# Optimization experiments

Measured on AMD Instinct MI355X. Metric: run time of the kernel, lower is better.

Reference implementation:

```python
import jax, jax.numpy as jnp
import numpy as np

EPS = 1e-4  # Coqui LayerNorm (type '1') eps


def _layer_norm_c(x, g, b):
    # x: (B, C, T); normalize over channel dim 1 (Coqui LayerNorm type '1')
    m = jnp.mean(x, axis=1, keepdims=True)
    v = jnp.var(x, axis=1, keepdims=True)
    return (x - m) * jax.lax.rsqrt(v + EPS) * g[None, :, None] + b[None, :, None]


def _s4d(x, log_dt, A_re, A_im, C_re, C_im, D, Wout, bout):
    # S4 (mode='diag' / S4D) layer, transposed=True -> x: (B, H, L)
    L = x.shape[-1]
    dt = jnp.exp(log_dt)[:, None]                       # (H, 1)
    A = A_re + 1j * A_im                                # (H, N2) diagonal SSM
    dtA = A * dt                                        # (H, N2)
    Cd = (C_re + 1j * C_im) * (jnp.exp(dtA) - 1.0) / A  # ZOH-discretized C (B absorbed)
    vand = jnp.exp(dtA[:, :, None] * jnp.arange(L))     # (H, N2, L) Vandermonde
    K = 2.0 * jnp.einsum('hn,hnl->hl', Cd, vand).real   # (H, L) SSM conv kernel
    n = 2 * L                                           # causal conv via FFT
    y = jnp.fft.irfft(jnp.fft.rfft(x, n=n) * jnp.fft.rfft(K, n=n)[None], n=n)[..., :L]
    y = y + D[None, :, None] * x                        # skip connection
    y = jax.nn.gelu(y, approximate=False)               # dropout=0 (eval)
    z = jnp.einsum('oh,bhl->bol', Wout, y) + bout[None, :, None]  # (B, 2H, L)
    a, g = jnp.split(z, 2, axis=1)                      # GLU over channel dim
    return a * jax.nn.sigmoid(g)


def _ffn(x, x_mask, W1, b1, W2, b2):
    # kernel_size=1 feed-forward conv block with masking
    h = jnp.einsum('fh,bhl->bfl', W1, x * x_mask) + b1[None, :, None]
    h = jax.nn.relu(h)
    o = jnp.einsum('of,bfl->bol', W2, h * x_mask) + b2[None, :, None]
    return o * x_mask


def reference(x, x_mask, log_dt, A_re, A_im, C_re, C_im, D, Wout, bout,
              g1, be1, W1, bf1, W2, bf2, g2, be2):
    n_layers = log_dt.shape[0]
    for i in range(n_layers):
        x = x * x_mask
        y = _s4d(x, log_dt[i], A_re[i], A_im[i], C_re[i], C_im[i],
                 D[i], Wout[i], bout[i])
        x = _layer_norm_c(x + y, g1[i], be1[i])
        y = _ffn(x, x_mask, W1[i], bf1[i], W2[i], bf2[i])
        x = _layer_norm_c(x + y, g2[i], be2[i])
    return x * x_mask


def setup_inputs():
    Lyr, B, H, T, N2, HF = 6, 16, 384, 2048, 32, 1536
    key = jax.random.key(0)
    ks = jax.random.split(key, 8)
    x = jax.random.normal(ks[0], (B, H, T), jnp.float32)
    x_mask = jnp.ones((B, 1, T), jnp.float32)
    # stable S4D init: log_dt in [log 1e-3, log 1e-1], A = -1/2 + i*pi*n
    log_dt = (jax.random.uniform(ks[1], (Lyr, H), jnp.float32)
              * (np.log(0.1) - np.log(0.001)) + np.log(0.001))
    A_re = -0.5 * jnp.ones((Lyr, H, N2), jnp.float32)
    A_im = jnp.broadcast_to(np.pi * jnp.arange(N2, dtype=np.float32),
                            (Lyr, H, N2)) * jnp.ones((1,), jnp.float32)
    C_re = jax.random.normal(ks[2], (Lyr, H, N2), jnp.float32) * 0.5 ** 0.5
    C_im = jax.random.normal(ks[3], (Lyr, H, N2), jnp.float32) * 0.5 ** 0.5
    D = jax.random.normal(ks[4], (Lyr, H), jnp.float32)
    Wout = jax.random.normal(ks[5], (Lyr, 2 * H, H), jnp.float32) / np.sqrt(H)
    bout = jnp.zeros((Lyr, 2 * H), jnp.float32)
    g1 = jnp.ones((Lyr, H), jnp.float32)
    be1 = jnp.zeros((Lyr, H), jnp.float32)
    W1 = jax.random.normal(ks[6], (Lyr, HF, H), jnp.float32) / np.sqrt(H)
    bf1 = jnp.zeros((Lyr, HF), jnp.float32)
    W2 = jax.random.normal(ks[7], (Lyr, H, HF), jnp.float32) / np.sqrt(HF)
    bf2 = jnp.zeros((Lyr, H), jnp.float32)
    g2 = jnp.ones((Lyr, H), jnp.float32)
    be2 = jnp.zeros((Lyr, H), jnp.float32)
    return {"x": x, "x_mask": x_mask, "log_dt": log_dt, "A_re": A_re,
            "A_im": A_im, "C_re": C_re, "C_im": C_im, "D": D,
            "Wout": Wout, "bout": bout, "g1": g1, "be1": be1,
            "W1": W1, "bf1": bf1, "W2": W2, "bf2": bf2,
            "g2": g2, "be2": be2}
```

## Files before the change

### kernel.cpp

```cpp
#include <hip/hip_runtime.h>
#include <math.h>

#define Bq 16
#define Hc 384
#define Tt 2048
#define N2 32
#define LYR 6
#define HFq 1536
#define TWOH 768
#define CHUNK 64
#define NCH (Tt/CHUNK)
#define NJ (Bq*NCH)
#define UH (NJ*CHUNK)

typedef __bf16 bf16x8 __attribute__((ext_vector_type(8)));
typedef float floatx4 __attribute__((ext_vector_type(4)));
typedef _Float16 f16_t;
typedef f16_t fp16x8 __attribute__((ext_vector_type(8)));
typedef f16_t fp16x4 __attribute__((ext_vector_type(4)));

__device__ __forceinline__ unsigned short bfbits(float f) {
  union { float f; unsigned u; } x; x.f = f;
  return (unsigned short)((x.u + 0x7FFF + ((x.u >> 16) & 1)) >> 16);
}
__device__ __forceinline__ float bf2f(unsigned short u) {
  union { unsigned u; float f; } x; x.u = ((unsigned)u) << 16; return x.f;
}

__device__ __forceinline__ void gl_lds16(const void* g, void* l) {
  __builtin_amdgcn_global_load_lds(
      (const __attribute__((address_space(1))) void*)g,
      (__attribute__((address_space(3))) void*)l, 16, 0, 0);
}

__global__ void param_kernel(const float* __restrict__ log_dt,
                             const float* __restrict__ A_re, const float* __restrict__ A_im,
                             const float* __restrict__ C_re, const float* __restrict__ C_im,
                             float* __restrict__ wre, float* __restrict__ wim,
                             float* __restrict__ cdre, float* __restrict__ cdim,
                             float* __restrict__ wSre, float* __restrict__ wSim) {
  int idx = blockIdx.x * blockDim.x + threadIdx.x;
  if (idx >= LYR * Hc * N2) return;
  int hn = idx / N2;
  double dt = exp((double)log_dt[hn]);
  double are = (double)A_re[idx], aim = (double)A_im[idx];
  double dre = are * dt, dimv = aim * dt;
  double er = exp(dre);
  double wr = er * cos(dimv), wi_ = er * sin(dimv);
  double den = are * are + aim * aim;
  double nr = wr - 1.0, ni = wi_;
  double qr = (nr * are + ni * aim) / den;
  double qi = (ni * are - nr * aim) / den;
  double cr = (double)C_re[idx], ci = (double)C_im[idx];
  cdre[idx] = (float)(2.0 * (cr * qr - ci * qi));
  cdim[idx] = (float)(2.0 * (cr * qi + ci * qr));
  wre[idx] = (float)wr; wim[idx] = (float)wi_;
  double es = exp(dre * (double)CHUNK);
  wSre[idx] = (float)(es * cos(dimv * (double)CHUNK));
  wSim[idx] = (float)(es * sin(dimv * (double)CHUNK));
}

__global__ void cvt_bf16_kernel(const float* __restrict__ in, unsigned short* __restrict__ out,
                                int n4) {
  int idx = blockIdx.x * 256 + threadIdx.x;
  if (idx >= n4) return;
  float4 v = ((const float4*)in)[idx];
  ushort4 o;
  o.x = bfbits(v.x); o.y = bfbits(v.y); o.z = bfbits(v.z); o.w = bfbits(v.w);
  ((ushort4*)out)[idx] = o;
}

__global__ __launch_bounds__(256) void transpose_fwd(const float* __restrict__ in,
                                                     float* __restrict__ out) {
  __shared__ float tile[32][33];
  int tx = threadIdx.x, ty = threadIdx.y;
  int t0 = blockIdx.x * 32, c0 = blockIdx.y * 32, b = blockIdx.z;
#pragma unroll
  for (int k = 0; k < 4; k++)
    tile[ty + 8 * k][tx] = in[((size_t)(b * Hc + c0 + ty + 8 * k)) * Tt + t0 + tx];
  __syncthreads();
#pragma unroll
  for (int k = 0; k < 4; k++)
    out[((size_t)(b * Tt + t0 + ty + 8 * k)) * Hc + c0 + tx] = tile[tx][ty + 8 * k];
}

__global__ __launch_bounds__(256) void transpose_bwd(const float* __restrict__ in,
                                                     const float* __restrict__ mask,
                                                     float* __restrict__ out) {
  __shared__ float tile[32][33];
  int tx = threadIdx.x, ty = threadIdx.y;
  int t0 = blockIdx.x * 32, c0 = blockIdx.y * 32, b = blockIdx.z;
#pragma unroll
  for (int k = 0; k < 4; k++)
    tile[ty + 8 * k][tx] = in[((size_t)(b * Tt + t0 + ty + 8 * k)) * Hc + c0 + tx];
  __syncthreads();
  float mv = mask[(size_t)b * Tt + t0 + tx];
#pragma unroll
  for (int k = 0; k < 4; k++)
    out[((size_t)(b * Hc + c0 + ty + 8 * k)) * Tt + t0 + tx] = tile[tx][ty + 8 * k] * mv;
}

__global__ __launch_bounds__(256) void pack_u(const float* __restrict__ xT,
                                              const float* __restrict__ mask,
                                              f16_t* __restrict__ U) {
  __shared__ float tile[64][65];
  int tid = threadIdx.x;
  int t0 = blockIdx.x * 64, h0 = blockIdx.y * 64, b = blockIdx.z;
#pragma unroll
  for (int p = 0; p < 4; p++) {
    int idx = p * 256 + tid;
    int row = idx >> 4, c4 = (idx & 15) * 4;
    float4 v = *(const float4*)&xT[((size_t)(b * Tt + t0 + row)) * Hc + h0 + c4];
    float mv = mask[(size_t)b * Tt + t0 + row];
    tile[row][c4] = v.x * mv; tile[row][c4 + 1] = v.y * mv;
    tile[row][c4 + 2] = v.z * mv; tile[row][c4 + 3] = v.w * mv;
  }
  __syncthreads();
#pragma unroll
  for (int p = 0; p < 2; p++) {
    int idx = p * 256 + tid;
    int hr = idx >> 3, g = (idx & 7) * 8;
    fp16x8 o;
#pragma unroll
    for (int i = 0; i < 8; i++) o[i] = (f16_t)tile[g + i][hr];
    *(fp16x8*)&U[(size_t)(h0 + hr) * UH + (size_t)b * Tt + t0 + g] = o;
  }
}

__global__ __launch_bounds__(256) void build_mats(
    const float* __restrict__ wre, const float* __restrict__ wim,
    const float* __restrict__ cdre, const float* __restrict__ cdim,
    f16_t* __restrict__ Ag, f16_t* __restrict__ Wg) {
  __shared__ float pre[65][32], pim[65][32], Kc[64], cdr_s[32], cdi_s[32];
  int h = blockIdx.x, tid = threadIdx.x;
  if (tid < 32) {
    float wr = wre[h * N2 + tid], wi = wim[h * N2 + tid];
    cdr_s[tid] = cdre[h * N2 + tid];
    cdi_s[tid] = cdim[h * N2 + tid];
    float pr = 1.f, pi = 0.f;
    for (int p = 0; p <= 64; p++) {
      pre[p][tid] = pr; pim[p][tid] = pi;
      float nr2 = pr * wr - pi * wi;
      pi = pr * wi + pi * wr;
      pr = nr2;
    }
  }
  __syncthreads();
  if (tid < 64) {
    float s = 0.f;
    for (int n = 0; n < 32; n++)
      s = fmaf(cdr_s[n], pre[tid][n], fmaf(-cdi_s[n], pim[tid][n], s));
    Kc[tid] = s;
  }
  __syncthreads();
  for (int i = tid; i < 64 * 128; i += 256) {
    int m = i >> 7, k = i & 127;
    float v;
    if (k < 64) {
      v = (m >= k) ? Kc[m - k] : 0.f;
    } else {
      int kk = k - 64, n = kk >> 1;
      v = (kk & 1) ? -fmaf(cdr_s[n], pim[m + 1][n], cdi_s[n] * pre[m + 1][n])
                   :  fmaf(cdr_s[n], pre[m + 1][n], -cdi_s[n] * pim[m + 1][n]);
    }
    Ag[(size_t)h * 8192 + i] = (f16_t)v;
  }
  for (int i = tid; i < 64 * 64; i += 256) {
    int m = i >> 6, tau = i & 63, n = m >> 1;
    float v = (m & 1) ? pim[63 - tau][n] : pre[63 - tau][n];
    Wg[(size_t)h * 4096 + i] = (f16_t)v;
  }
}

__global__ __launch_bounds__(256) void gemm_state(const f16_t* __restrict__ U,
                                                  const f16_t* __restrict__ Wg,
                                                  f16_t* __restrict__ St) {
  __shared__ f16_t Aw[64][72];
  __shared__ f16_t Bu[128][72];
  int tid = threadIdx.x;
  int j0 = blockIdx.x * 128, h = blockIdx.y;
#pragma unroll
  for (int p = 0; p < 2; p++) {
    int idx = p * 256 + tid;
    int row = idx >> 3, c8 = (idx & 7) * 8;
    *(fp16x8*)&Aw[row][c8] = *(const fp16x8*)&Wg[(size_t)h * 4096 + row * 64 + c8];
  }
#pragma unroll
  for (int p = 0; p < 4; p++) {
    int idx = p * 256 + tid;
    int row = idx >> 3, c8 = (idx & 7) * 8;
    *(fp16x8*)&Bu[row][c8] =
        *(const fp16x8*)&U[(size_t)h * UH + (size_t)(j0 + row) * CHUNK + c8];
  }
  __syncthreads();
  int wave = tid >> 6, lane = tid & 63, l16 = lane & 15, quad = lane >> 4;
  int m0 = wave * 16;
  floatx4 acc[8];
#pragma unroll
  for (int jt = 0; jt < 8; jt++) acc[jt] = (floatx4){0.f, 0.f, 0.f, 0.f};
#pragma unroll
  for (int kk = 0; kk < 2; kk++) {
    fp16x8 a = *(const fp16x8*)&Aw[m0 + l16][kk * 32 + quad * 8];
#pragma unroll
    for (int jt = 0; jt < 8; jt++) {
      fp16x8 bb = *(const fp16x8*)&Bu[jt * 16 + l16][kk * 32 + quad * 8];
      acc[jt] = __builtin_amdgcn_mfma_f32_16x16x32_f16(a, bb, acc[jt], 0, 0, 0);
    }
  }
#pragma unroll
  for (int jt = 0; jt < 8; jt++) {
    int j = j0 + jt * 16 + l16;
    fp16x4 o;
#pragma unroll
    for (int r = 0; r < 4; r++) o[r] = (f16_t)acc[jt][r];
    *(fp16x4*)&St[(size_t)h * UH + (size_t)j * CHUNK + m0 + quad * 4] = o;
  }
}

__global__ __launch_bounds__(256) void scan_prefix2(
    f16_t* __restrict__ St,
    const float* __restrict__ wSre, const float* __restrict__ wSim) {
  int gid = blockIdx.x * 256 + threadIdx.x;
  if (gid >= Hc * Bq * N2) return;
  int n = gid & 31;
  int b = (gid >> 5) & 15;
  int h = gid >> 9;
  float wr = wSre[h * N2 + n], wi = wSim[h * N2 + n];
  float cr = 0.f, ci = 0.f;
  unsigned* base = (unsigned*)(St + (size_t)h * UH + (size_t)b * Tt + 2 * n);
  for (int c = 0; c < NCH; c++) {
    union { unsigned u; f16_t h2[2]; } in, out;
    in.u = base[c * 32];
    float sre = (float)in.h2[0], sim = (float)in.h2[1];
    out.h2[0] = (f16_t)cr; out.h2[1] = (f16_t)ci;
    base[c * 32] = out.u;
    float c0 = cr;
    cr = fmaf(wr, c0, fmaf(-wi, ci, sre));
    ci = fmaf(wr, ci, fmaf(wi, c0, sim));
  }
}

__global__ __launch_bounds__(256) void gemm_out(
    const f16_t* __restrict__ U, const f16_t* __restrict__ Ag,
    const f16_t* __restrict__ St, const float* __restrict__ Dv,
    unsigned short* __restrict__ Yb) {
  __shared__ f16_t Aa[64][136];
  __shared__ f16_t Bb[128][136];
  int tid = threadIdx.x;
  int j0 = blockIdx.x * 128, h = blockIdx.y;
#pragma unroll
  for (int p = 0; p < 4; p++) {
    int idx = p * 256 + tid;
    int row = idx >> 4, c8 = (idx & 15) * 8;
    *(fp16x8*)&Aa[row][c8] = *(const fp16x8*)&Ag[(size_t)h * 8192 + row * 128 + c8];
  }
#pragma unroll
  for (int p = 0; p < 4; p++) {
    int idx = p * 256 + tid;
    int row = idx >> 3, c8 = (idx & 7) * 8;
    *(fp16x8*)&Bb[row][c8] =
        *(const fp16x8*)&U[(size_t)h * UH + (size_t)(j0 + row) * CHUNK + c8];
    *(fp16x8*)&Bb[row][64 + c8] =
        *(const fp16x8*)&St[(size_t)h * UH + (size_t)(j0 + row) * CHUNK + c8];
  }
  __syncthreads();
  int wave = tid >> 6, lane = tid & 63, l16 = lane & 15, quad = lane >> 4;
  int m0 = wave * 16;
  floatx4 acc[8];
#pragma unroll
  for (int jt = 0; jt < 8; jt++) acc[jt] = (floatx4){0.f, 0.f, 0.f, 0.f};
#pragma unroll
  for (int kk = 0; kk < 4; kk++) {
    fp16x8 a = *(const fp16x8*)&Aa[m0 + l16][kk * 32 + quad * 8];
#pragma unroll
    for (int jt = 0; jt < 8; jt++) {
      fp16x8 bb = *(const fp16x8*)&Bb[jt * 16 + l16][kk * 32 + quad * 8];
      acc[jt] = __builtin_amdgcn_mfma_f32_16x16x32_f16(a, bb, acc[jt], 0, 0, 0);
    }
  }
  float d = Dv[h];
  int tb = m0 + quad * 4;
#pragma unroll
  for (int jt = 0; jt < 8; jt++) {
    int jr = jt * 16 + l16;
    fp16x4 u4 = *(const fp16x4*)&Bb[jr][tb];
    ushort4 o;
#pragma unroll
    for (int r = 0; r < 4; r++) {
      float v = fmaf(d, (float)u4[r], acc[jt][r]);
      v = 0.5f * v * (1.0f + erff(v * 0.70710678118654752f));
      ((unsigned short*)&o)[r] = bfbits(v);
    }
    *(ushort4*)&Yb[(size_t)h * UH + (size_t)(j0 + jr) * CHUNK + tb] = o;
  }
}

__global__ __launch_bounds__(256) void unpack_y(const unsigned short* __restrict__ Yb,
                                                unsigned short* __restrict__ yb) {
  __shared__ unsigned short tile[64][65];
  int tid = threadIdx.x;
  int t0 = blockIdx.x * 64, h0 = blockIdx.y * 64, b = blockIdx.z;
#pragma unroll
  for (int p = 0; p < 2; p++) {
    int idx = p * 256 + tid;
    int hr = idx >> 3, g = (idx & 7) * 8;
    uint4 v = *(const uint4*)&Yb[(size_t)(h0 + hr) * UH + (size_t)b * Tt + t0 + g];
    const unsigned short* s = (const unsigned short*)&v;
#pragma unroll
    for (int i = 0; i < 8; i++) tile[hr][g + i] = s[i];
  }
  __syncthreads();
#pragma unroll
  for (int p = 0; p < 2; p++) {
    int idx = p * 256 + tid;
    int tr = idx >> 3, g = (idx & 7) * 8;
    unsigned short o[8];
#pragma unroll
    for (int i = 0; i < 8; i++) o[i] = tile[g + i][tr];
    *(uint4*)&yb[((size_t)(b * Tt + t0 + tr)) * Hc + h0 + g] = *(uint4*)o;
  }
}

template <int EPI>
__global__ __launch_bounds__(256) void mfma_gemm(
    const __bf16* __restrict__ act, const __bf16* __restrict__ W,
    const float* __restrict__ bias, const float* __restrict__ mask,
    unsigned short* __restrict__ outb, int K, int NOUT) {
  __shared__ __bf16 As[2][128][32];
  __shared__ __bf16 Bs[2][128][32];
  __shared__ __bf16 Bs2[(EPI == 2) ? 2 : 1][(EPI == 2) ? 128 : 1][32];
  int tid = threadIdx.x;
  int b = blockIdx.z;
  int t0 = blockIdx.x * 128, n0 = blockIdx.y * 128;
  int wave = tid >> 6, lane = tid & 63, l16 = lane & 15, quad = lane >> 4;
  int wm = wave >> 1, wn = wave & 1;

  floatx4 acc[4][4];
  floatx4 accg[(EPI == 2) ? 4 : 1][4];
#pragma unroll
  for (int i = 0; i < 4; i++)
#pragma unroll
    for (int j = 0; j < 4; j++) {
      acc[i][j] = (floatx4){0.f, 0.f, 0.f, 0.f};
      if constexpr (EPI == 2) accg[i][j] = (floatx4){0.f, 0.f, 0.f, 0.f};
    }

  int srow = wave * 16 + (lane >> 2);
  int scol = (lane & 3) * 8;
  const __bf16* aSrc = act + ((size_t)(b * Tt + t0 + srow)) * K + scol;
  const __bf16* bSrc = W + (size_t)(n0 + srow) * K + scol;
  const __bf16* gSrc = W + (size_t)(NOUT + n0 + srow) * K + scol;

  auto stage = [&](int buf, int k0) {
#pragma unroll
    for (int r = 0; r < 2; r++) {
      gl_lds16(aSrc + k0 + (size_t)(64 * r) * K, &As[buf][wave * 16 + r * 64][0]);
      gl_lds16(bSrc + k0 + (size_t)(64 * r) * K, &Bs[buf][wave * 16 + r * 64][0]);
      if constexpr (EPI == 2)
        gl_lds16(gSrc + k0 + (size_t)(64 * r) * K, &Bs2[buf][wave * 16 + r * 64][0]);
    }
  };

  stage(0, 0);
  __syncthreads();
  int cur = 0;
  for (int k0 = 0; k0 < K; k0 += 32) {
    if (k0 + 32 < K) stage(cur ^ 1, k0 + 32);
    bf16x8 af[4], bfr[4], gfr[(EPI == 2) ? 4 : 1];
#pragma unroll
    for (int i = 0; i < 4; i++)
      af[i] = *(const bf16x8*)&As[cur][wm * 64 + i * 16 + l16][quad * 8];
#pragma unroll
    for (int j = 0; j < 4; j++) {
      bfr[j] = *(const bf16x8*)&Bs[cur][wn * 64 + j * 16 + l16][quad * 8];
      if constexpr (EPI == 2)
        gfr[j] = *(const bf16x8*)&Bs2[cur][wn * 64 + j * 16 + l16][quad * 8];
    }
#pragma unroll
    for (int i = 0; i < 4; i++)
#pragma unroll
      for (int j = 0; j < 4; j++) {
        acc[i][j] = __builtin_amdgcn_mfma_f32_16x16x32_bf16(af[i], bfr[j], acc[i][j], 0, 0, 0);
        if constexpr (EPI == 2)
          accg[i][j] = __builtin_amdgcn_mfma_f32_16x16x32_bf16(af[i], gfr[j], accg[i][j], 0, 0, 0);
      }
    __syncthreads();
    cur ^= 1;
  }

#pragma unroll
  for (int i = 0; i < 4; i++) {
    int tb = t0 + wm * 64 + i * 16 + quad * 4;
    float mv[4];
    if constexpr (EPI == 1) {
#pragma unroll
      for (int r = 0; r < 4; r++) mv[r] = mask[(size_t)b * Tt + tb + r];
    }
#pragma unroll
    for (int j = 0; j < 4; j++) {
      int n = n0 + wn * 64 + j * 16 + l16;
      float bn = bias[n];
      float bg = (EPI == 2) ? bias[NOUT + n] : 0.f;
#pragma unroll
      for (int r = 0; r < 4; r++) {
        size_t o = ((size_t)(b * Tt + tb + r)) * NOUT + n;
        if constexpr (EPI == 0) {
          outb[o] = bfbits(acc[i][j][r] + bn);
        } else if constexpr (EPI == 1) {
          float v = fmaxf(acc[i][j][r] + bn, 0.f) * mv[r];
          outb[o] = bfbits(v);
        } else {
          float a = acc[i][j][r] + bn;
          float g = accg[i][j][r] + bg;
          outb[o] = bfbits(a / (1.f + expf(-g)));
        }
      }
    }
  }
}

__global__ __launch_bounds__(256) void ln_t(
    const float* __restrict__ in1, const unsigned short* __restrict__ in2b,
    const float* __restrict__ mask, const float* __restrict__ gamma,
    const float* __restrict__ beta, float* __restrict__ out,
    unsigned short* __restrict__ outb, int m1, int m2) {
  int row = blockIdx.x * 4 + (threadIdx.x >> 6);
  int lane = threadIdx.x & 63;
  float mv = mask[row];
  float f1 = m1 ? mv : 1.f;
  float f2 = m2 ? mv : 1.f;
  size_t base = (size_t)row * Hc;
  float v[6], sum = 0.f, sq = 0.f;
#pragma unroll
  for (int j = 0; j < 6; j++) {
    int idx = lane + 64 * j;
    float a = in1[base + idx] * f1 + bf2f(in2b[base + idx]) * f2;
    v[j] = a; sum += a; sq = fmaf(a, a, sq);
  }
#pragma unroll
  for (int off = 32; off >= 1; off >>= 1) {
    sum += __shfl_xor(sum, off, 64);
    sq  += __shfl_xor(sq,  off, 64);
  }
  float m = sum * (1.f / Hc);
  float var = sq * (1.f / Hc) - m * m;
  float rs = rsqrtf(var + 1e-4f);
#pragma unroll
  for (int j = 0; j < 6; j++) {
    int idx = lane + 64 * j;
    float o = (v[j] - m) * rs * gamma[idx] + beta[idx];
    out[base + idx] = o;
    if (outb) outb[base + idx] = bfbits(o * mv);
  }
}

__global__ void diag_kernel(float* out, float v) {
  if (blockIdx.x == 0 && threadIdx.x == 0) out[0] = v;
}

extern "C" void kernel_launch(void* const* d_in, const int* in_sizes, int n_in,
                              void* d_out, int out_size, void* d_ws, size_t ws_size,
                              hipStream_t stream) {
  const float* x_in  = (const float*)d_in[0];
  const float* xmask = (const float*)d_in[1];
  const float* log_dt = (const float*)d_in[2];
  const float* A_re = (const float*)d_in[3];
  const float* A_im = (const float*)d_in[4];
  const float* C_re = (const float*)d_in[5];
  const float* C_im = (const float*)d_in[6];
  const float* Dv   = (const float*)d_in[7];
  const float* Wout = (const float*)d_in[8];
  const float* bout = (const float*)d_in[9];
  const float* g1   = (const float*)d_in[10];
  const float* be1  = (const float*)d_in[11];
  const float* W1   = (const float*)d_in[12];
  const float* bf1  = (const float*)d_in[13];
  const float* W2   = (const float*)d_in[14];
  const float* bf2  = (const float*)d_in[15];
  const float* g2   = (const float*)d_in[16];
  const float* be2  = (const float*)d_in[17];

  const size_t NXf   = (size_t)Bq * Hc * Tt;
  const size_t NP    = (size_t)LYR * Hc * N2;
  const size_t YBFf  = NXf / 2;
  const size_t HBFf  = (size_t)Bq * Tt * HFq / 2;
  const size_t WOUTf = (size_t)LYR * TWOH * Hc / 2;
  const size_t W1f   = (size_t)LYR * HFq * Hc / 2;
  const size_t W2f   = (size_t)LYR * Hc * HFq / 2;

  size_t need = 2 * NXf + YBFf + HBFf + WOUTf + W1f + W2f + 6 * NP;
  if (ws_size / 4 < need) {
    diag_kernel<<<1, 64, 0, stream>>>((float*)d_out, 1000.0f + (float)(ws_size >> 20));
    return;
  }

  float* ws = (float*)d_ws;
  float* xT   = ws;
  float* tmp  = xT + NXf;
  float* ybfF = tmp + NXf;
  float* hbfF = ybfF + YBFf;
  float* wobF = hbfF + HBFf;
  float* w1bF = wobF + WOUTf;
  float* w2bF = w1bF + W1f;
  float* wre  = w2bF + W2f;
  float* wim  = wre + NP;
  float* cdre = wim + NP;
  float* cdim = cdre + NP;
  float* wSre = cdim + NP;
  float* wSim = wSre + NP;

  unsigned short* ybf = (unsigned short*)ybfF;
  unsigned short* hbf = (unsigned short*)hbfF;
  unsigned short* wob = (unsigned short*)wobF;
  unsigned short* w1b = (unsigned short*)w1bF;
  unsigned short* w2b = (unsigned short*)w2bF;
  float* x1 = (float*)d_out;

  f16_t* Ub   = (f16_t*)tmp;
  unsigned short* tmpb = (unsigned short*)(tmp + NXf / 2);
  f16_t* St16 = (f16_t*)hbfF;
  unsigned short* Ybi = (unsigned short*)(hbfF + YBFf);
  f16_t* Ag   = (f16_t*)(hbfF + 2 * YBFf);
  f16_t* Wg   = Ag + (size_t)384 * 8192;

  param_kernel<<<(LYR * Hc * N2 + 255) / 256, 256, 0, stream>>>(
      log_dt, A_re, A_im, C_re, C_im, wre, wim, cdre, cdim, wSre, wSim);
  cvt_bf16_kernel<<<(int)(2 * WOUTf + 1023) / 1024, 256, 0, stream>>>(Wout, wob, (int)(WOUTf / 2));
  cvt_bf16_kernel<<<(int)(2 * W1f + 1023) / 1024, 256, 0, stream>>>(W1, w1b, (int)(W1f / 2));
  cvt_bf16_kernel<<<(int)(2 * W2f + 1023) / 1024, 256, 0, stream>>>(W2, w2b, (int)(W2f / 2));
  transpose_fwd<<<dim3(Tt / 32, Hc / 32, Bq), dim3(32, 8), 0, stream>>>(x_in, xT);

  for (int i = 0; i < LYR; i++) {
    size_t po = (size_t)i * Hc * N2;

    pack_u<<<dim3(Tt / 64, Hc / 64, Bq), 256, 0, stream>>>(xT, xmask, Ub);
    build_mats<<<Hc, 256, 0, stream>>>(wre + po, wim + po, cdre + po, cdim + po, Ag, Wg);
    gemm_state<<<dim3(NJ / 128, Hc), 256, 0, stream>>>(Ub, Wg, St16);
    scan_prefix2<<<(Hc * Bq * N2) / 256, 256, 0, stream>>>(St16, wSre + po, wSim + po);
    gemm_out<<<dim3(NJ / 128, Hc), 256, 0, stream>>>(Ub, Ag, St16, Dv + (size_t)i * Hc, Ybi);
    unpack_y<<<dim3(Tt / 64, Hc / 64, Bq), 256, 0, stream>>>(Ybi, ybf);

    mfma_gemm<2><<<dim3(Tt / 128, Hc / 128, Bq), 256, 0, stream>>>(
        (const __bf16*)ybf, (const __bf16*)(wob + (size_t)i * TWOH * Hc),
        bout + (size_t)i * TWOH, xmask, tmpb, Hc, Hc);

    ln_t<<<(Bq * Tt) / 4, 256, 0, stream>>>(
        xT, tmpb, xmask, g1 + (size_t)i * Hc, be1 + (size_t)i * Hc, x1, ybf, 1, 0);

    mfma_gemm<1><<<dim3(Tt / 128, HFq / 128, Bq), 256, 0, stream>>>(
        (const __bf16*)ybf, (const __bf16*)(w1b + (size_t)i * HFq * Hc),
        bf1 + (size_t)i * HFq, xmask, hbf, Hc, HFq);

    mfma_gemm<0><<<dim3(Tt / 128, Hc / 128, Bq), 256, 0, stream>>>(
        (const __bf16*)hbf, (const __bf16*)(w2b + (size_t)i * Hc * HFq),
        bf2 + (size_t)i * Hc, xmask, tmpb, HFq, Hc);

    ln_t<<<(Bq * Tt) / 4, 256, 0, stream>>>(
        x1, tmpb, xmask, g2 + (size_t)i * Hc, be2 + (size_t)i * Hc, xT, nullptr, 0, 1);
  }

  transpose_bwd<<<dim3(Tt / 32, Hc / 32, Bq), dim3(32, 8), 0, stream>>>(xT, xmask, (float*)d_out);
}
```

Measured before the change: 1.901 ms.

## Triple-buffer GEMM LDS staging with XOR swizzle and single barrier per K-step

Converts the MFMA GEMM from double to triple buffering, so global-to-LDS loads run two K-tiles ahead. The old end-of-iteration __syncthreads is replaced by an explicit vmcnt wait plus one s_barrier per step. It also XOR-swizzles LDS column placement on both the store and read side to reduce bank conflicts on the fragment loads. The cost is more LDS per block, which may lower occupancy, and the hand-written vmcnt counts must match the number of outstanding loads, so correctness is fragile.

```diff
diff --git a/kernel.cpp b/kernel.cpp
--- a/kernel.cpp
+++ b/kernel.cpp
@@ -326,9 +326,9 @@
     const __bf16* __restrict__ act, const __bf16* __restrict__ W,
     const float* __restrict__ bias, const float* __restrict__ mask,
     unsigned short* __restrict__ outb, int K, int NOUT) {
-  __shared__ __bf16 As[2][128][32];
-  __shared__ __bf16 Bs[2][128][32];
-  __shared__ __bf16 Bs2[(EPI == 2) ? 2 : 1][(EPI == 2) ? 128 : 1][32];
+  __shared__ __bf16 As[3][128][32];
+  __shared__ __bf16 Bs[3][128][32];
+  __shared__ __bf16 Bs2[(EPI == 2) ? 3 : 1][(EPI == 2) ? 128 : 1][32];
   int tid = threadIdx.x;
   int b = blockIdx.z;
   int t0 = blockIdx.x * 128, n0 = blockIdx.y * 128;
@@ -346,7 +346,7 @@
     }
 
   int srow = wave * 16 + (lane >> 2);
-  int scol = (lane & 3) * 8;
+  int scol = (((lane & 3) ^ ((lane >> 3) & 3)) * 8);
   const __bf16* aSrc = act + ((size_t)(b * Tt + t0 + srow)) * K + scol;
   const __bf16* bSrc = W + (size_t)(n0 + srow) * K + scol;
   const __bf16* gSrc = W + (size_t)(NOUT + n0 + srow) * K + scol;
@@ -361,21 +361,33 @@
     }
   };
 
+  const int NT = K >> 5;
+  int swz = (quad ^ ((l16 >> 1) & 3)) << 4;
   stage(0, 0);
-  __syncthreads();
-  int cur = 0;
-  for (int k0 = 0; k0 < K; k0 += 32) {
-    if (k0 + 32 < K) stage(cur ^ 1, k0 + 32);
+  stage(1, 32);
+  for (int t = 0; t < NT; ++t) {
+    if (t + 1 < NT) {
+      asm volatile("s_waitcnt vmcnt(%0)" :: "i"((EPI == 2) ? 6 : 4) : "memory");
+    } else {
+      asm volatile("s_waitcnt vmcnt(0)" ::: "memory");
+    }
+    __builtin_amdgcn_s_barrier();
+    __builtin_amdgcn_sched_barrier(0);
+    int cur = t % 3;
     bf16x8 af[4], bfr[4], gfr[(EPI == 2) ? 4 : 1];
 #pragma unroll
     for (int i = 0; i < 4; i++)
-      af[i] = *(const bf16x8*)&As[cur][wm * 64 + i * 16 + l16][quad * 8];
+      af[i] = *(const bf16x8*)((const char*)&As[cur][0][0] +
+                               (wm * 64 + i * 16 + l16) * 64 + swz);
 #pragma unroll
     for (int j = 0; j < 4; j++) {
-      bfr[j] = *(const bf16x8*)&Bs[cur][wn * 64 + j * 16 + l16][quad * 8];
+      bfr[j] = *(const bf16x8*)((const char*)&Bs[cur][0][0] +
+                                (wn * 64 + j * 16 + l16) * 64 + swz);
       if constexpr (EPI == 2)
-        gfr[j] = *(const bf16x8*)&Bs2[cur][wn * 64 + j * 16 + l16][quad * 8];
-    }
+        gfr[j] = *(const bf16x8*)((const char*)&Bs2[cur][0][0] +
+                                  (wn * 64 + j * 16 + l16) * 64 + swz);
+    }
+    if (t + 2 < NT) stage((t + 2) % 3, (t + 2) * 32);
 #pragma unroll
     for (int i = 0; i < 4; i++)
 #pragma unroll
@@ -384,8 +396,6 @@
         if constexpr (EPI == 2)
           accg[i][j] = __builtin_amdgcn_mfma_f32_16x16x32_bf16(af[i], gfr[j], accg[i][j], 0, 0, 0);
       }
-    __syncthreads();
-    cur ^= 1;
   }
 
 #pragma unroll
```

Result: faster. 1.843 ms (-3.0%).
